# Optimization experiments

Measured on AMD Instinct MI355X. Metric: run time of the kernel, lower is better.

Reference implementation:

```python
import jax, jax.numpy as jnp
import numpy as np

BATCH, TIMESTEPS, DIM, OUT = 64, 512, 1024, 1024


def setup_inputs() -> dict:
    key = jax.random.key(0)
    k1, k2, k3, k4, k5, k6 = jax.random.split(key, 6)
    # glorot-normal-ish scales for params
    def glorot(k, shape):
        fan_in, fan_out = shape[0], shape[-1]
        std = (2.0 / (fan_in + fan_out)) ** 0.5
        return jax.random.normal(k, shape, dtype=jnp.float32) * std
    return {
        "inputs": jax.random.normal(k1, (BATCH, TIMESTEPS, DIM), dtype=jnp.float32),
        "prev_state": jax.random.normal(k2, (BATCH, OUT), dtype=jnp.float32),
        "Wa": glorot(k3, (OUT, OUT)),
        "Ua": glorot(k4, (DIM, OUT)),
        "Va": glorot(k5, (OUT, 1)),
        "Ba": glorot(k6, (1, OUT)),
    }


def reference(inputs, prev_state, Wa, Ua, Va, Ba):
    # WaS: [B, 1, OUT] broadcast over timesteps
    WaS = jnp.einsum("bo,op->bp", prev_state, Wa)[:, None, :]
    # UaH: [B, T, OUT]
    UaH = jnp.einsum("btd,do->bto", inputs, Ua)
    scores = jnp.tanh(UaH + WaS + Ba)            # [B, T, OUT]
    scores = jax.nn.relu(scores @ Va)            # [B, T, 1]
    sm = jax.nn.softmax(scores, axis=1)          # softmax over timesteps
    context_vector = jnp.sum(inputs * sm, axis=1)  # [B, DIM]
    return context_vector
```

## Files before the change

### kernel.cpp

```cpp
#include <hip/hip_runtime.h>


#define NBATCH 64
#define NT     512
#define NDIM   1024
#define NOUT   1024

typedef _Float16 h8 __attribute__((ext_vector_type(8)));
typedef _Float16 h4 __attribute__((ext_vector_type(4)));
typedef float f16v __attribute__((ext_vector_type(16)));

__device__ __forceinline__ float tanh_fast(float x) {
    float e = __expf(2.0f * x);
    return 1.0f - 2.0f * __builtin_amdgcn_rcpf(e + 1.0f);
}

__global__ __launch_bounds__(256) void k_pack_ua(const float* __restrict__ Ua,
                                                 _Float16* __restrict__ B16) {
    int t = blockIdx.x * 256 + threadIdx.x;
    int nn = t & 31, kg = (t >> 5) & 1, ks = (t >> 6) & 63, nt = t >> 12;
    int n = (nt << 5) + nn;
    int kbase = (ks << 4) + (kg << 3);
    h8 v;
#pragma unroll
    for (int j = 0; j < 8; ++j) v[j] = (_Float16)Ua[(size_t)(kbase + j) * 1024 + n];
    *(h8*)(B16 + ((size_t)t << 3)) = v;
}

__global__ __launch_bounds__(256) void k_was_part(const float* __restrict__ ps,
                                                  const float* __restrict__ Wa,
                                                  float* __restrict__ part) {
    int oc = blockIdx.x, b = blockIdx.y, tid = threadIdx.x;
    const float4* Wa4 = (const float4*)Wa;
    const float* psb = ps + b * 1024;
    float4 acc = {0.f, 0.f, 0.f, 0.f};
    int o0 = oc * 64;
#pragma unroll 4
    for (int o = o0; o < o0 + 64; ++o) {
        float s = psb[o];
        float4 wv = Wa4[o * 256 + tid];
        acc.x += s * wv.x; acc.y += s * wv.y; acc.z += s * wv.z; acc.w += s * wv.w;
    }
    ((float4*)part)[((oc << 6) + b) * 256 + tid] = acc;
}

__global__ __launch_bounds__(256) void k_was_reduce(const float* __restrict__ part,
                                                    const float* __restrict__ Ba,
                                                    float* __restrict__ wsWaS) {
    int b = blockIdx.x, tid = threadIdx.x;
    const float4* p4 = (const float4*)part;
    float4 acc = ((const float4*)Ba)[tid];
#pragma unroll
    for (int oc = 0; oc < 16; ++oc) {
        float4 v = p4[((oc << 6) + b) * 256 + tid];
        acc.x += v.x; acc.y += v.y; acc.z += v.z; acc.w += v.w;
    }
    ((float4*)wsWaS)[b * 256 + tid] = acc;
}

#define ASH_STRIDE 136
__global__ __launch_bounds__(512, 4) void k_fused_gemm(
    const float* __restrict__ inputs, const _Float16* __restrict__ B16,
    const float* __restrict__ wsWaS, const float* __restrict__ Va,
    float* __restrict__ scores)
{
    __shared__ _Float16 Ash[2][64 * ASH_STRIDE];
    __shared__ float scoreSh[64];
    const int tid = threadIdx.x;
    const int lane = tid & 63, wv = tid >> 6;
    const int l31 = lane & 31, lhi = lane >> 5;
    const int r0 = blockIdx.x * 64;
    const int b = r0 >> 9;
    const int srow = tid >> 3, sq = tid & 7;
    const float4* srcBase = (const float4*)inputs + (size_t)(r0 + srow) * 256 + sq * 4;

    if (tid < 64) scoreSh[tid] = 0.0f;

    float4 vA[4];
#pragma unroll
    for (int j = 0; j < 4; ++j) vA[j] = srcBase[j];
    {
        _Float16* dst = &Ash[0][srow * ASH_STRIDE + sq * 16];
#pragma unroll
        for (int j = 0; j < 4; ++j) {
            float4 v = vA[j];
            *(h4*)(dst + j * 4) =
                (h4){ (_Float16)v.x, (_Float16)v.y, (_Float16)v.z, (_Float16)v.w };
        }
    }
    __syncthreads();

    for (int pass = 0; pass < 2; ++pass) {
        const int c0w = pass * 512 + wv * 64;
        const int ntb = c0w >> 5;
        f16v acc[2][2];
#pragma unroll
        for (int rt = 0; rt < 2; ++rt)
#pragma unroll
            for (int ct = 0; ct < 2; ++ct)
#pragma unroll
                for (int e = 0; e < 16; ++e) acc[rt][ct][e] = 0.0f;

        for (int kc = 0; kc < 8; ++kc) {
            const int buf = kc & 1;
            const bool pf = !(pass == 1 && kc == 7);
            if (pf) {
                const float4* src = srcBase + (((kc + 1) & 7) << 5);
#pragma unroll
                for (int j = 0; j < 4; ++j) vA[j] = src[j];
            }
#pragma unroll
            for (int ks8 = 0; ks8 < 8; ++ks8) {
                const int ks = kc * 8 + ks8;
                h8 a0 = *(const h8*)&Ash[buf][l31 * ASH_STRIDE + ks8 * 16 + lhi * 8];
                h8 a1 = *(const h8*)&Ash[buf][(32 + l31) * ASH_STRIDE + ks8 * 16 + lhi * 8];
                h8 bf[2];
#pragma unroll
                for (int ct = 0; ct < 2; ++ct)
                    bf[ct] = *(const h8*)(B16 +
                        ((size_t)(((ntb + ct) << 6) + ks) << 9) + lane * 8);
#pragma unroll
                for (int ct = 0; ct < 2; ++ct) {
                    acc[0][ct] = __builtin_amdgcn_mfma_f32_32x32x16_f16(a0, bf[ct], acc[0][ct], 0, 0, 0);
                    acc[1][ct] = __builtin_amdgcn_mfma_f32_32x32x16_f16(a1, bf[ct], acc[1][ct], 0, 0, 0);
                }
            }
            if (pf) {
                _Float16* dst = &Ash[buf ^ 1][srow * ASH_STRIDE + sq * 16];
#pragma unroll
                for (int j = 0; j < 4; ++j) {
                    float4 v = vA[j];
                    *(h4*)(dst + j * 4) =
                        (h4){ (_Float16)v.x, (_Float16)v.y, (_Float16)v.z, (_Float16)v.w };
                }
            }
            __syncthreads();
        }
        float wsv[2], vav[2];
#pragma unroll
        for (int ct = 0; ct < 2; ++ct) {
            int n = c0w + ct * 32 + l31;
            wsv[ct] = wsWaS[b * 1024 + n];
            vav[ct] = Va[n];
        }
#pragma unroll
        for (int rt = 0; rt < 2; ++rt) {
#pragma unroll
            for (int i = 0; i < 16; ++i) {
                float s = 0.0f;
#pragma unroll
                for (int ct = 0; ct < 2; ++ct)
                    s += tanh_fast(acc[rt][ct][i] + wsv[ct]) * vav[ct];
                s += __shfl_xor(s, 1);
                s += __shfl_xor(s, 2);
                s += __shfl_xor(s, 4);
                s += __shfl_xor(s, 8);
                s += __shfl_xor(s, 16);
                if (l31 == 0) {
                    int row = rt * 32 + (i & 3) + ((i >> 2) << 3) + (lhi << 2);
                    atomicAdd(&scoreSh[row], s);
                }
            }
        }
    }
    __syncthreads();
    if (tid < 64) scores[r0 + tid] = fmaxf(scoreSh[tid], 0.0f);
}

__global__ __launch_bounds__(256) void k_softmax(const float* __restrict__ scores,
                                                 float* __restrict__ sm) {
    int b = blockIdx.x, tid = threadIdx.x;
    __shared__ float red[256];
    const float* sb = scores + b * 512;
    float s0 = sb[tid], s1 = sb[tid + 256];
    red[tid] = fmaxf(s0, s1);
    __syncthreads();
    for (int st = 128; st > 0; st >>= 1) {
        if (tid < st) red[tid] = fmaxf(red[tid], red[tid + st]);
        __syncthreads();
    }
    float m = red[0];
    __syncthreads();
    float e0 = __expf(s0 - m), e1 = __expf(s1 - m);
    red[tid] = e0 + e1;
    __syncthreads();
    for (int st = 128; st > 0; st >>= 1) {
        if (tid < st) red[tid] += red[tid + st];
        __syncthreads();
    }
    float inv = 1.0f / red[0];
    sm[b * 512 + tid] = e0 * inv;
    sm[b * 512 + 256 + tid] = e1 * inv;
}

__global__ __launch_bounds__(256) void k_ctx_part(const float* __restrict__ inputs,
                                                  const float* __restrict__ sm,
                                                  float* __restrict__ part) {
    int ts = blockIdx.x, b = blockIdx.y, tid = threadIdx.x;
    const float4* inF4 = (const float4*)inputs;
    float4 acc = {0.f, 0.f, 0.f, 0.f};
    int t0 = ts * 32;
#pragma unroll 8
    for (int t = t0; t < t0 + 32; ++t) {
        float wgt = sm[b * 512 + t];
        float4 x = inF4[(size_t)(b * 512 + t) * 256 + tid];
        acc.x += wgt * x.x; acc.y += wgt * x.y; acc.z += wgt * x.z; acc.w += wgt * x.w;
    }
    ((float4*)part)[((ts << 6) + b) * 256 + tid] = acc;
}

__global__ __launch_bounds__(256) void k_ctx_reduce(const float* __restrict__ part,
                                                    float* __restrict__ out) {
    int g = blockIdx.x * 256 + threadIdx.x;
    const float4* p4 = (const float4*)part;
    float4 acc = p4[g];
#pragma unroll
    for (int s = 1; s < 16; ++s) {
        float4 v = p4[s * 16384 + g];
        acc.x += v.x; acc.y += v.y; acc.z += v.z; acc.w += v.w;
    }
    ((float4*)out)[g] = acc;
}

extern "C" void kernel_launch(void* const* d_in, const int* in_sizes, int n_in,
                              void* d_out, int out_size, void* d_ws, size_t ws_size,
                              hipStream_t stream) {
    const float* inputs = (const float*)d_in[0];
    const float* prev   = (const float*)d_in[1];
    const float* Wa     = (const float*)d_in[2];
    const float* Ua     = (const float*)d_in[3];
    const float* Va     = (const float*)d_in[4];
    const float* Ba     = (const float*)d_in[5];
    float* out = (float*)d_out;

    char* ws = (char*)d_ws;
    _Float16* B16   = (_Float16*)(ws);
    float* wasPart  = (float*)(ws + (2u << 20));
    float* wsWaS    = (float*)(ws + (6u << 20));
    float* scores   = (float*)(ws + (6u << 20) + (256u << 10));
    float* sm       = (float*)(ws + (6u << 20) + (384u << 10));
    float* ctxPart  = (float*)(ws);

    hipLaunchKernelGGL(k_pack_ua,    dim3(512),    dim3(256), 0, stream, Ua, B16);
    hipLaunchKernelGGL(k_was_part,   dim3(16, 64), dim3(256), 0, stream, prev, Wa, wasPart);
    hipLaunchKernelGGL(k_was_reduce, dim3(64),     dim3(256), 0, stream, wasPart, Ba, wsWaS);
    hipLaunchKernelGGL(k_fused_gemm, dim3(512),    dim3(512), 0, stream, inputs, B16, wsWaS, Va, scores);
    hipLaunchKernelGGL(k_softmax,    dim3(64),     dim3(256), 0, stream, scores, sm);
    hipLaunchKernelGGL(k_ctx_part,   dim3(16, 64), dim3(256), 0, stream, inputs, sm, ctxPart);
    hipLaunchKernelGGL(k_ctx_reduce, dim3(64),     dim3(256), 0, stream, ctxPart, out);
}
```

Baseline: 343.1 us.

## Restructure fused GEMM to single pass with 64x128 warp tiles and swizzled LDS

The fused score GEMM now runs in one pass instead of two. Each wave owns 128 output columns (4 column tiles), so each A fragment read from LDS feeds twice as many MFMAs. The A tile is loaded as two halves of K (512 each) into a single XOR-swizzled LDS buffer rather than double-buffered 128-wide chunks, which cuts the number of barriers. B fragments are prefetched four k-steps ahead in registers. This trades higher register pressure (launch bounds drop occupancy to 2 blocks) and larger LDS use for less LDS traffic, fewer syncs and better B-load latency hiding, but global A loads are no longer overlapped with compute.

```diff
diff --git a/kernel.cpp b/kernel.cpp
--- a/kernel.cpp
+++ b/kernel.cpp
@@ -58,13 +58,12 @@
     ((float4*)wsWaS)[b * 256 + tid] = acc;
 }
 
-#define ASH_STRIDE 136
-__global__ __launch_bounds__(512, 4) void k_fused_gemm(
+__global__ __launch_bounds__(512, 2) void k_fused_gemm(
     const float* __restrict__ inputs, const _Float16* __restrict__ B16,
     const float* __restrict__ wsWaS, const float* __restrict__ Va,
     float* __restrict__ scores)
 {
-    __shared__ _Float16 Ash[2][64 * ASH_STRIDE];
+    __shared__ _Float16 Ash[64 * 512];
     __shared__ float scoreSh[64];
     const int tid = threadIdx.x;
     const int lane = tid & 63, wv = tid >> 6;
@@ -72,94 +71,95 @@
     const int r0 = blockIdx.x * 64;
     const int b = r0 >> 9;
     const int srow = tid >> 3, sq = tid & 7;
-    const float4* srcBase = (const float4*)inputs + (size_t)(r0 + srow) * 256 + sq * 4;
 
     if (tid < 64) scoreSh[tid] = 0.0f;
 
-    float4 vA[4];
-#pragma unroll
-    for (int j = 0; j < 4; ++j) vA[j] = srcBase[j];
-    {
-        _Float16* dst = &Ash[0][srow * ASH_STRIDE + sq * 16];
-#pragma unroll
-        for (int j = 0; j < 4; ++j) {
-            float4 v = vA[j];
-            *(h4*)(dst + j * 4) =
-                (h4){ (_Float16)v.x, (_Float16)v.y, (_Float16)v.z, (_Float16)v.w };
+    const int ntb = wv << 2;
+    const _Float16* bBase = B16 + ((size_t)ntb << 15) + lane * 8;
+
+    f16v acc[2][4];
+#pragma unroll
+    for (int rt = 0; rt < 2; ++rt)
+#pragma unroll
+        for (int ct = 0; ct < 4; ++ct)
+#pragma unroll
+            for (int e = 0; e < 16; ++e) acc[rt][ct][e] = 0.0f;
+
+    h8 bp[4][4];
+#pragma unroll
+    for (int s = 0; s < 4; ++s)
+#pragma unroll
+        for (int ct = 0; ct < 4; ++ct)
+            bp[s][ct] = *(const h8*)(bBase + ((size_t)ct << 15) + ((size_t)s << 9));
+
+    const int aswz = (l31 & 7) << 4;
+    int aoff[4];
+#pragma unroll
+    for (int s = 0; s < 4; ++s) aoff[s] = (32 * s + 16 * lhi) ^ aswz;
+    const char* a0b = (const char*)Ash + l31 * 1024;
+    const char* a1b = a0b + 32 * 1024;
+    const int swz = (srow & 7) << 4;
+
+#pragma unroll
+    for (int h = 0; h < 2; ++h) {
+        if (h == 1) __syncthreads();
+        {
+            const float4* src = (const float4*)inputs +
+                                (size_t)(r0 + srow) * 256 + (h << 7) + sq;
+            char* rowb = (char*)Ash + srow * 1024;
+#pragma unroll 8
+            for (int jj = 0; jj < 16; ++jj) {
+                float4 v = src[jj * 8];
+                *(h4*)(rowb + ((64 * jj + 8 * sq) ^ swz)) =
+                    (h4){ (_Float16)v.x, (_Float16)v.y, (_Float16)v.z, (_Float16)v.w };
+            }
         }
-    }
-    __syncthreads();
-
-    for (int pass = 0; pass < 2; ++pass) {
-        const int c0w = pass * 512 + wv * 64;
-        const int ntb = c0w >> 5;
-        f16v acc[2][2];
-#pragma unroll
-        for (int rt = 0; rt < 2; ++rt)
-#pragma unroll
-            for (int ct = 0; ct < 2; ++ct)
-#pragma unroll
-                for (int e = 0; e < 16; ++e) acc[rt][ct][e] = 0.0f;
-
-        for (int kc = 0; kc < 8; ++kc) {
-            const int buf = kc & 1;
-            const bool pf = !(pass == 1 && kc == 7);
-            if (pf) {
-                const float4* src = srcBase + (((kc + 1) & 7) << 5);
-#pragma unroll
-                for (int j = 0; j < 4; ++j) vA[j] = src[j];
-            }
-#pragma unroll
-            for (int ks8 = 0; ks8 < 8; ++ks8) {
-                const int ks = kc * 8 + ks8;
-                h8 a0 = *(const h8*)&Ash[buf][l31 * ASH_STRIDE + ks8 * 16 + lhi * 8];
-                h8 a1 = *(const h8*)&Ash[buf][(32 + l31) * ASH_STRIDE + ks8 * 16 + lhi * 8];
-                h8 bf[2];
-#pragma unroll
-                for (int ct = 0; ct < 2; ++ct)
-                    bf[ct] = *(const h8*)(B16 +
-                        ((size_t)(((ntb + ct) << 6) + ks) << 9) + lane * 8);
-#pragma unroll
-                for (int ct = 0; ct < 2; ++ct) {
-                    acc[0][ct] = __builtin_amdgcn_mfma_f32_32x32x16_f16(a0, bf[ct], acc[0][ct], 0, 0, 0);
-                    acc[1][ct] = __builtin_amdgcn_mfma_f32_32x32x16_f16(a1, bf[ct], acc[1][ct], 0, 0, 0);
+        __syncthreads();
+
+        for (int ks4 = 0; ks4 < 8; ++ks4) {
+#pragma unroll
+            for (int s = 0; s < 4; ++s) {
+                const int ks = (h << 5) + ks4 * 4 + s;
+                h8 a0 = *(const h8*)(a0b + ks4 * 128 + aoff[s]);
+                h8 a1 = *(const h8*)(a1b + ks4 * 128 + aoff[s]);
+#pragma unroll
+                for (int ct = 0; ct < 4; ++ct) {
+                    acc[0][ct] = __builtin_amdgcn_mfma_f32_32x32x16_f16(a0, bp[s][ct], acc[0][ct], 0, 0, 0);
+                    acc[1][ct] = __builtin_amdgcn_mfma_f32_32x32x16_f16(a1, bp[s][ct], acc[1][ct], 0, 0, 0);
+                }
+                if (h == 0 || ks4 < 7) {
+#pragma unroll
+                    for (int ct = 0; ct < 4; ++ct)
+                        bp[s][ct] = *(const h8*)(bBase + ((size_t)ct << 15) +
+                                                 ((size_t)(ks + 4) << 9));
                 }
             }
-            if (pf) {
-                _Float16* dst = &Ash[buf ^ 1][srow * ASH_STRIDE + sq * 16];
-#pragma unroll
-                for (int j = 0; j < 4; ++j) {
-                    float4 v = vA[j];
-                    *(h4*)(dst + j * 4) =
-                        (h4){ (_Float16)v.x, (_Float16)v.y, (_Float16)v.z, (_Float16)v.w };
-                }
-            }
-            __syncthreads();
         }
-        float wsv[2], vav[2];
-#pragma unroll
-        for (int ct = 0; ct < 2; ++ct) {
-            int n = c0w + ct * 32 + l31;
-            wsv[ct] = wsWaS[b * 1024 + n];
-            vav[ct] = Va[n];
-        }
-#pragma unroll
-        for (int rt = 0; rt < 2; ++rt) {
-#pragma unroll
-            for (int i = 0; i < 16; ++i) {
-                float s = 0.0f;
-#pragma unroll
-                for (int ct = 0; ct < 2; ++ct)
-                    s += tanh_fast(acc[rt][ct][i] + wsv[ct]) * vav[ct];
-                s += __shfl_xor(s, 1);
-                s += __shfl_xor(s, 2);
-                s += __shfl_xor(s, 4);
-                s += __shfl_xor(s, 8);
-                s += __shfl_xor(s, 16);
-                if (l31 == 0) {
-                    int row = rt * 32 + (i & 3) + ((i >> 2) << 3) + (lhi << 2);
-                    atomicAdd(&scoreSh[row], s);
-                }
+    }
+
+    float wsv[4], vav[4];
+#pragma unroll
+    for (int ct = 0; ct < 4; ++ct) {
+        int n = (wv << 7) + ct * 32 + l31;
+        wsv[ct] = wsWaS[b * 1024 + n];
+        vav[ct] = Va[n];
+    }
+#pragma unroll
+    for (int rt = 0; rt < 2; ++rt) {
+#pragma unroll
+        for (int i = 0; i < 16; ++i) {
+            float s = 0.0f;
+#pragma unroll
+            for (int ct = 0; ct < 4; ++ct)
+                s += tanh_fast(acc[rt][ct][i] + wsv[ct]) * vav[ct];
+            s += __shfl_xor(s, 1);
+            s += __shfl_xor(s, 2);
+            s += __shfl_xor(s, 4);
+            s += __shfl_xor(s, 8);
+            s += __shfl_xor(s, 16);
+            if (l31 == 0) {
+                int row = rt * 32 + (i & 3) + ((i >> 2) << 3) + (lhi << 2);
+                atomicAdd(&scoreSh[row], s);
             }
         }
     }
```

After: 330.3 us. 3.7% less time.
